# Kernel tuning notes

Measured on AMD Instinct MI355X. Metric: run time of the kernel, lower is better.

Reference implementation:

```python
import jax, jax.numpy as jnp
import numpy as np

B, SEED, GEN = 32, 128, 384
IN, H, OUT = 171, 1024, 171


def setup_inputs() -> dict:
    key = jax.random.key(0)
    ks = jax.random.split(key, 16)
    s = 0.05
    w = lambda k, shape: (jax.random.normal(k, shape, jnp.float32) * s)
    inp = {
        "seed_seq": jax.random.normal(ks[0], (B, SEED, IN), jnp.float32),
        "Wih1": w(ks[1], (4 * H, IN)),  "Whh1": w(ks[2], (4 * H, H)),
        "bih1": w(ks[3], (4 * H,)),     "bhh1": w(ks[4], (4 * H,)),
        "Wih2": w(ks[5], (4 * H, H)),   "Whh2": w(ks[6], (4 * H, H)),
        "bih2": w(ks[7], (4 * H,)),     "bhh2": w(ks[8], (4 * H,)),
        "Wih3": w(ks[9], (4 * H, H)),   "Whh3": w(ks[10], (4 * H, H)),
        "bih3": w(ks[11], (4 * H,)),    "bhh3": w(ks[12], (4 * H,)),
        "Wdec": w(ks[13], (OUT, H)),    "bdec": w(ks[14], (OUT,)),
        "gen_len": GEN,
    }
    return inp


def _lstm_cell(x, h, c, Wih, Whh, bih, bhh):
    # PyTorch LSTMCell: gate order i, f, g, o
    gates = x @ Wih.T + bih + h @ Whh.T + bhh  # [B, 4H]
    i, f, g, o = jnp.split(gates, 4, axis=-1)
    c_new = jax.nn.sigmoid(f) * c + jax.nn.sigmoid(i) * jnp.tanh(g)
    h_new = jax.nn.sigmoid(o) * jnp.tanh(c_new)
    return h_new, c_new


def reference(seed_seq, Wih1, Whh1, bih1, bhh1, Wih2, Whh2, bih2, bhh2,
              Wih3, Whh3, bih3, bhh3, Wdec, bdec, gen_len):
    batch = seed_seq.shape[0]
    hsz = Whh1.shape[1]
    z = jnp.zeros((batch, hsz), seed_seq.dtype)

    def step(state, x):
        h1, c1, h2, c2, h3, c3 = state
        h1, c1 = _lstm_cell(x, h1, c1, Wih1, Whh1, bih1, bhh1)
        h2, c2 = _lstm_cell(h1, h2, c2, Wih2, Whh2, bih2, bhh2)
        h3, c3 = _lstm_cell(h2, h3, c3, Wih3, Whh3, bih3, bhh3)
        out = h3 @ Wdec.T + bdec
        return (h1, c1, h2, c2, h3, c3), out

    # conditioning (seed) phase: scan over time-major seed sequence
    state0 = (z, z, z, z, z, z)
    state, seed_outs = jax.lax.scan(step, state0, jnp.swapaxes(seed_seq, 0, 1))

    def gen_step(carry, _):
        cur, st = carry
        st, out = step(st, cur)
        return (out, st), out

    _, gen_outs = jax.lax.scan(gen_step, (seed_outs[-1], state), None, length=gen_len)

    outs = jnp.concatenate([seed_outs, gen_outs], axis=0)  # [T, B, OUT]
    return jnp.swapaxes(outs, 0, 1)  # [B, T, OUT]
```

## Files before the change

### kernel.cpp

```cpp
#include <hip/hip_runtime.h>
#include <hip/hip_bf16.h>
#include <math.h>

#define NB    32
#define NSEED 128
#define NTT   512
#define NIN   171
#define NINP  192
#define NH    1024
#define NG    4096
#define NOUT  171
#define NOUTP 176
#define NWG   256

typedef unsigned short u16;
typedef unsigned int u32;
typedef __attribute__((ext_vector_type(8))) short bf16x8;
typedef __attribute__((ext_vector_type(4))) float f32x4;

__device__ __host__ inline u16 f2bf(float x) {
  union { float f; unsigned u; } v; v.f = x;
  unsigned r = v.u + 0x7FFFu + ((v.u >> 16) & 1u);
  return (u16)(r >> 16);
}

__global__ void pack_mat(const float* __restrict__ src, u16* __restrict__ dst, int ktiles) {
  int id = blockIdx.x * 256 + threadIdx.x;
  int total = ktiles * 256 * 64;
  if (id >= total) return;
  int lane = id & 63;
  int nt = (id >> 6) & 255;
  int kt = id >> 14;
  int c = lane & 15, q = lane >> 4;
  int r = (c & 3) * 1024 + nt * 4 + (c >> 2);
  int K = ktiles * 32;
  const float* s = src + (size_t)r * K + kt * 32 + q * 8;
  __attribute__((aligned(16))) u16 o[8];
#pragma unroll
  for (int j = 0; j < 8; ++j) o[j] = f2bf(s[j]);
  *(bf16x8*)(dst + (size_t)id * 8) = *(const bf16x8*)o;
}

__global__ void pack_wih1(const float* __restrict__ src, u16* __restrict__ dst) {
  int id = blockIdx.x * 256 + threadIdx.x;
  if (id >= 6 * 256 * 64) return;
  int lane = id & 63;
  int nt = (id >> 6) & 255;
  int kt = id >> 14;
  int c = lane & 15, q = lane >> 4;
  int r = (c & 3) * 1024 + nt * 4 + (c >> 2);
  int k0 = kt * 32 + q * 8;
  __attribute__((aligned(16))) u16 o[8];
#pragma unroll
  for (int j = 0; j < 8; ++j) {
    int k = k0 + j;
    o[j] = (k < NIN) ? f2bf(src[(size_t)r * NIN + k]) : (u16)0;
  }
  *(bf16x8*)(dst + (size_t)id * 8) = *(const bf16x8*)o;
}

__global__ void pack_wdec(const float* __restrict__ src, u16* __restrict__ dst) {
  int id = blockIdx.x * 256 + threadIdx.x;
  if (id >= 32 * 11 * 64) return;
  int lane = id & 63;
  int nt = (id >> 6) % 11;
  int kt = (id >> 6) / 11;
  int c = lane & 15, q = lane >> 4;
  int r = nt * 16 + c;
  int k0 = kt * 32 + q * 8;
  __attribute__((aligned(16))) u16 o[8];
#pragma unroll
  for (int j = 0; j < 8; ++j) {
    o[j] = (r < NOUT) ? f2bf(src[(size_t)r * NH + k0 + j]) : (u16)0;
  }
  *(bf16x8*)(dst + (size_t)id * 8) = *(const bf16x8*)o;
}

__global__ void pack_seed(const float* __restrict__ src, u16* __restrict__ dst) {
  int id = blockIdx.x * 256 + threadIdx.x;
  if (id >= NSEED * NB * NINP) return;
  int kp = id % NINP;
  int b = (id / NINP) % NB;
  int t = id / (NINP * NB);
  float v = (kp < NIN) ? src[((size_t)b * NSEED + t) * NIN + kp] : 0.f;
  dst[id] = f2bf(v);
}

__global__ void wfuse_kernel(const float* __restrict__ wih1, const float* __restrict__ wdec,
                             float* __restrict__ tmp) {
  int n = blockIdx.x;
  int k = blockIdx.y * 256 + threadIdx.x;
  const float* wr = wih1 + (size_t)n * NIN;
  float s = 0.f;
  for (int i = 0; i < NIN; ++i) s += wr[i] * wdec[(size_t)i * NH + k];
  tmp[(size_t)n * NH + k] = s;
}

__global__ void prep_bias(const float* bih1, const float* bhh1, const float* bih2, const float* bhh2,
                          const float* bih3, const float* bhh3, const float* __restrict__ wih1,
                          const float* __restrict__ bdec_in,
                          float* b1s, float* b1g, float* b2, float* b3, float* bdecp) {
  int n = blockIdx.x * 256 + threadIdx.x;
  if (n >= NG) return;
  int wgi = n >> 4, c = n & 15;
  int r = (c & 3) * 1024 + wgi * 4 + (c >> 2);
  float v1 = bih1[r] + bhh1[r];
  b1s[n] = v1;
  float bf = 0.f;
  for (int i = 0; i < NIN; ++i) bf += wih1[(size_t)r * NIN + i] * bdec_in[i];
  b1g[n] = v1 + bf;
  b2[n] = bih2[r] + bhh2[r];
  b3[n] = bih3[r] + bhh3[r];
  if (n < NOUTP) bdecp[n] = (n < NOUT) ? bdec_in[n] : 0.f;
}

__device__ __forceinline__ void load16_sc1(bf16x8 (&a0)[8], bf16x8 (&a1)[8],
                                           const u16* b0, const u16* b1) {
  asm volatile(
      "global_load_dwordx4 %0, %16, off sc0 sc1\n\t"
      "global_load_dwordx4 %8, %17, off sc0 sc1\n\t"
      "global_load_dwordx4 %1, %16, off offset:256 sc0 sc1\n\t"
      "global_load_dwordx4 %9, %17, off offset:256 sc0 sc1\n\t"
      "global_load_dwordx4 %2, %16, off offset:512 sc0 sc1\n\t"
      "global_load_dwordx4 %10, %17, off offset:512 sc0 sc1\n\t"
      "global_load_dwordx4 %3, %16, off offset:768 sc0 sc1\n\t"
      "global_load_dwordx4 %11, %17, off offset:768 sc0 sc1\n\t"
      "global_load_dwordx4 %4, %16, off offset:1024 sc0 sc1\n\t"
      "global_load_dwordx4 %12, %17, off offset:1024 sc0 sc1\n\t"
      "global_load_dwordx4 %5, %16, off offset:1280 sc0 sc1\n\t"
      "global_load_dwordx4 %13, %17, off offset:1280 sc0 sc1\n\t"
      "global_load_dwordx4 %6, %16, off offset:1536 sc0 sc1\n\t"
      "global_load_dwordx4 %14, %17, off offset:1536 sc0 sc1\n\t"
      "global_load_dwordx4 %7, %16, off offset:1792 sc0 sc1\n\t"
      "global_load_dwordx4 %15, %17, off offset:1792 sc0 sc1\n\t"
      "s_waitcnt vmcnt(0)"
      : "=&v"(a0[0]), "=&v"(a0[1]), "=&v"(a0[2]), "=&v"(a0[3]),
        "=&v"(a0[4]), "=&v"(a0[5]), "=&v"(a0[6]), "=&v"(a0[7]),
        "=&v"(a1[0]), "=&v"(a1[1]), "=&v"(a1[2]), "=&v"(a1[3]),
        "=&v"(a1[4]), "=&v"(a1[5]), "=&v"(a1[6]), "=&v"(a1[7])
      : "v"(b0), "v"(b1)
      : "memory");
}

#define MFMA_BF16 __builtin_amdgcn_mfma_f32_16x16x32_bf16

__device__ __forceinline__ void mm32_lds(f32x4& d0, f32x4& d1, const u16* wl,
                                         const u16* x, int wv, int lane) {
  int m = lane & 15, q = lane >> 4;
  const u16* xa = x + m * NH + q * 8 + wv * 32;
  const u16* xb = xa + 16 * NH;
  bf16x8 a0[8], a1[8];
  load16_sc1(a0, a1, xa, xb);
  const u16* wb = wl + lane * 8;
#pragma unroll
  for (int i = 0; i < 8; ++i) {
    bf16x8 w = *(const bf16x8*)(wb + (size_t)(wv + 4 * i) * 512);
    d0 = MFMA_BF16(a0[i], w, d0, 0, 0, 0);
    d1 = MFMA_BF16(a1[i], w, d1, 0, 0, 0);
  }
}

__device__ __forceinline__ void mm32_glb(f32x4& d0, f32x4& d1, const u16* wgb,
                                         const u16* x, int wv, int lane) {
  int m = lane & 15, q = lane >> 4;
  const u16* xa = x + m * NH + q * 8 + wv * 32;
  const u16* xb = xa + 16 * NH;
  const u16* wb = wgb + lane * 8;
  bf16x8 w[8];
#pragma unroll
  for (int i = 0; i < 8; ++i) w[i] = *(const bf16x8*)(wb + (size_t)(wv + 4 * i) * 131072);
  bf16x8 a0[8], a1[8];
  load16_sc1(a0, a1, xa, xb);
#pragma unroll
  for (int i = 0; i < 8; ++i) {
    d0 = MFMA_BF16(a0[i], w[i], d0, 0, 0, 0);
    d1 = MFMA_BF16(a1[i], w[i], d1, 0, 0, 0);
  }
}

__device__ __forceinline__ void mm6_glb(f32x4& d0, f32x4& d1, const u16* __restrict__ wbase,
                                        const u16* __restrict__ x, int wv, int lane) {
  int m = lane & 15, q = lane >> 4;
  const u16* xa = x + m * NINP + q * 8;
  const u16* xb = xa + 16 * NINP;
  const u16* wb = wbase + lane * 8;
#pragma unroll
  for (int i = 0; i < 2; ++i) {
    int kt = wv + 4 * i;
    if (kt >= 6) break;
    bf16x8 w = *(const bf16x8*)(wb + (size_t)kt * 131072);
    bf16x8 a0 = *(const bf16x8*)(xa + kt * 32);
    bf16x8 a1 = *(const bf16x8*)(xb + kt * 32);
    d0 = MFMA_BF16(a0, w, d0, 0, 0, 0);
    d1 = MFMA_BF16(a1, w, d1, 0, 0, 0);
  }
}

__global__ __launch_bounds__(256, 1) void lstm_main(
    const u16* __restrict__ whh1, const u16* __restrict__ whh2, const u16* __restrict__ whh3,
    const u16* __restrict__ wih2, const u16* __restrict__ wih3,
    const u16* __restrict__ wfuse, const u16* __restrict__ wih1,
    const u16* __restrict__ seedp,
    u16* __restrict__ h1b, u16* __restrict__ h2b, u16* __restrict__ h3h,
    const float* __restrict__ b1s, const float* __restrict__ b1g,
    const float* __restrict__ b2, const float* __restrict__ b3,
    int* __restrict__ flags)
{
  __shared__ u16  wlds[3 * 16384];
  __shared__ float red[4][64][8];
  __shared__ float gbuf[32][16];
  __shared__ float cst[3][32][4];

  int wg = blockIdx.x;
  int tid = threadIdx.x;
  int wv = tid >> 6, lane = tid & 63;

  {
    const u16* srcs[3] = { wih2 + (size_t)wg * 512, wih3 + (size_t)wg * 512,
                           wfuse + (size_t)wg * 512 };
#pragma unroll
    for (int m = 0; m < 3; ++m) {
      for (int i = tid; i < 2048; i += 256) {
        int kt = i >> 6, ln = i & 63;
        *(bf16x8*)&wlds[m * 16384 + (kt * 64 + ln) * 8] =
            *(const bf16x8*)(srcs[m] + ((size_t)kt * 16384 + ln) * 8);
      }
    }
    float* cp = &cst[0][0][0];
    for (int i = tid; i < 3 * 32 * 4; i += 256) cp[i] = 0.f;
  }
  __syncthreads();

  int c0 = tid & 15;
  float bv_s  = b1s[wg * 16 + c0];
  float bv_g  = b1g[wg * 16 + c0];
  float bv_2  = b2 [wg * 16 + c0];
  float bv_3  = b3 [wg * 16 + c0];

  const u16* whhg[3] = { whh1 + (size_t)wg * 512, whh2 + (size_t)wg * 512,
                         whh3 + (size_t)wg * 512 };
  const u16* wih1g = wih1 + (size_t)wg * 512;

  int ep = 0;
  for (int t = 0; t < NTT; ++t) {
    int par = t & 1, parp = par ^ 1;
    for (int l = 0; l < 3; ++l) {
      f32x4 d0 = {0.f, 0.f, 0.f, 0.f}, d1 = {0.f, 0.f, 0.f, 0.f};
      bool isseed = (t < NSEED);

      if (l == 0 && isseed)
        mm6_glb(d0, d1, wih1g, seedp + (size_t)t * NB * NINP, wv, lane);
      if (t > 0) {
        const u16* hs = (l == 0) ? h1b + (size_t)parp * NB * NH
                     : (l == 1) ? h2b + (size_t)parp * NB * NH
                                : h3h + (size_t)(t - 1) * NB * NH;
        mm32_glb(d0, d1, whhg[l], hs, wv, lane);
      }

      bool skipwait = (l == 0 && isseed);
      if (ep > 0 && !skipwait) {
        if (tid < 64) {
          const int* fp = flags + (tid << 2);
          for (;;) {
            int f0 = __hip_atomic_load(fp + 0, __ATOMIC_RELAXED, __HIP_MEMORY_SCOPE_AGENT);
            int f1 = __hip_atomic_load(fp + 1, __ATOMIC_RELAXED, __HIP_MEMORY_SCOPE_AGENT);
            int f2 = __hip_atomic_load(fp + 2, __ATOMIC_RELAXED, __HIP_MEMORY_SCOPE_AGENT);
            int f3 = __hip_atomic_load(fp + 3, __ATOMIC_RELAXED, __HIP_MEMORY_SCOPE_AGENT);
            int mn = min(min(f0, f1), min(f2, f3));
            if (__all(mn >= ep)) break;
            __builtin_amdgcn_s_sleep(1);
          }
        }
        __syncthreads();
      }

      if (l == 0) {
        if (!isseed)
          mm32_lds(d0, d1, &wlds[2 * 16384], h3h + (size_t)(t - 1) * NB * NH, wv, lane);
      } else {
        const u16* xs = (l == 1) ? h1b + (size_t)par * NB * NH
                                 : h2b + (size_t)par * NB * NH;
        mm32_lds(d0, d1, &wlds[(l - 1) * 16384], xs, wv, lane);
      }

#pragma unroll
      for (int r = 0; r < 4; ++r) { red[wv][lane][r] = d0[r]; red[wv][lane][4 + r] = d1[r]; }
      __syncthreads();
      {
        int c = tid & 15, brow = tid >> 4;
        float bv = (l == 0) ? (isseed ? bv_s : bv_g) : (l == 1) ? bv_2 : bv_3;
        int srcl = ((brow >> 2) << 4) | c;
#pragma unroll
        for (int mt = 0; mt < 2; ++mt) {
          int b = brow + mt * 16;
          int idx = mt * 4 + (brow & 3);
          gbuf[b][c] = red[0][srcl][idx] + red[1][srcl][idx] +
                       red[2][srcl][idx] + red[3][srcl][idx] + bv;
        }
      }
      __syncthreads();

      if (tid < 128) {
        int b = tid & 31, jl = tid >> 5;
        float gi = gbuf[b][jl * 4 + 0], gf = gbuf[b][jl * 4 + 1];
        float gg = gbuf[b][jl * 4 + 2], go = gbuf[b][jl * 4 + 3];
        float si = 1.f / (1.f + expf(-gi));
        float sf = 1.f / (1.f + expf(-gf));
        float so = 1.f / (1.f + expf(-go));
        float cn = sf * cst[l][b][jl] + si * tanhf(gg);
        cst[l][b][jl] = cn;
        float hn = so * tanhf(cn);
        unsigned hv = (unsigned)f2bf(hn);
        unsigned other = (unsigned)__shfl_xor((int)hv, 32, 64);
        if (lane < 32) {
          unsigned val = hv | (other << 16);
          int w01 = tid >> 6;
          u16* hdst = (l == 0) ? h1b + (size_t)par * NB * NH
                    : (l == 1) ? h2b + (size_t)par * NB * NH
                               : h3h + (size_t)t * NB * NH;
          u32* hp = (u32*)hdst + (size_t)b * 512 + wg * 2 + w01;
          __hip_atomic_store(hp, val, __ATOMIC_RELAXED, __HIP_MEMORY_SCOPE_AGENT);
        }
      }

      __syncthreads();
      ++ep;
      if (tid == 0)
        __hip_atomic_store(&flags[wg], ep, __ATOMIC_RELAXED, __HIP_MEMORY_SCOPE_AGENT);
    }
  }
}

__global__ __launch_bounds__(256) void dec_kernel(
    const u16* __restrict__ h3h, const u16* __restrict__ wdec,
    const float* __restrict__ bdecp, float* __restrict__ out)
{
  int task = blockIdx.x * 4 + (threadIdx.x >> 6);
  int lane = threadIdx.x & 63;
  int nt = task % 11, rt = task / 11;
  if (rt >= NTT) return;
  int m = lane & 15, q = lane >> 4;
  const u16* xa = h3h + ((size_t)rt * 32 + m) * NH + q * 8;
  const u16* xb = xa + (size_t)16 * NH;
  f32x4 d0 = {0.f, 0.f, 0.f, 0.f}, d1 = {0.f, 0.f, 0.f, 0.f};
  for (int kt = 0; kt < 32; ++kt) {
    bf16x8 bf = *(const bf16x8*)(wdec + ((size_t)(kt * 11 + nt) * 64 + lane) * 8);
    bf16x8 a0 = *(const bf16x8*)(xa + kt * 32);
    bf16x8 a1 = *(const bf16x8*)(xb + kt * 32);
    d0 = MFMA_BF16(a0, bf, d0, 0, 0, 0);
    d1 = MFMA_BF16(a1, bf, d1, 0, 0, 0);
  }
  int o = nt * 16 + m;
  if (o >= NOUT) return;
  float bv = bdecp[o];
#pragma unroll
  for (int reg = 0; reg < 4; ++reg) {
    int row0 = rt * 32 + q * 4 + reg;
    out[(((size_t)(row0 & 31)) * NTT + (row0 >> 5)) * NOUT + o] = d0[reg] + bv;
    int row1 = row0 + 16;
    out[(((size_t)(row1 & 31)) * NTT + (row1 >> 5)) * NOUT + o] = d1[reg] + bv;
  }
}

extern "C" void kernel_launch(void* const* d_in, const int* in_sizes, int n_in,
                              void* d_out, int out_size, void* d_ws, size_t ws_size,
                              hipStream_t stream) {
  const float* seed = (const float*)d_in[0];
  const float* Wih1 = (const float*)d_in[1];
  const float* Whh1 = (const float*)d_in[2];
  const float* bih1 = (const float*)d_in[3];
  const float* bhh1 = (const float*)d_in[4];
  const float* Wih2 = (const float*)d_in[5];
  const float* Whh2 = (const float*)d_in[6];
  const float* bih2 = (const float*)d_in[7];
  const float* bhh2 = (const float*)d_in[8];
  const float* Wih3 = (const float*)d_in[9];
  const float* Whh3 = (const float*)d_in[10];
  const float* bih3 = (const float*)d_in[11];
  const float* bhh3 = (const float*)d_in[12];
  const float* Wdec = (const float*)d_in[13];
  const float* bdec = (const float*)d_in[14];

  char* ws = (char*)d_ws;
  size_t off = 0;
  auto alloc = [&](size_t bytes) -> void* {
    void* p = ws + off;
    off += (bytes + 63) & ~(size_t)63;
    return p;
  };
  const size_t BIGPK = (size_t)32 * 256 * 64 * 8 * 2;
  u16* whh1p  = (u16*)alloc(BIGPK);
  u16* whh2p  = (u16*)alloc(BIGPK);
  u16* whh3p  = (u16*)alloc(BIGPK);
  u16* wih2p  = (u16*)alloc(BIGPK);
  u16* wih3p  = (u16*)alloc(BIGPK);
  u16* wfusep = (u16*)alloc(BIGPK);
  u16* wih1p  = (u16*)alloc((size_t)6 * 256 * 64 * 8 * 2);
  u16* wdecp  = (u16*)alloc((size_t)32 * 11 * 64 * 8 * 2);
  u16* seedp  = (u16*)alloc((size_t)NSEED * NB * NINP * 2);
  u16* h1b    = (u16*)alloc((size_t)2 * NB * NH * 2);
  u16* h2b    = (u16*)alloc((size_t)2 * NB * NH * 2);
  u16* h3h    = (u16*)alloc((size_t)NTT * NB * NH * 2);
  float* b1s  = (float*)alloc((size_t)NG * 4);
  float* b1g  = (float*)alloc((size_t)NG * 4);
  float* b2   = (float*)alloc((size_t)NG * 4);
  float* b3   = (float*)alloc((size_t)NG * 4);
  float* bdecp = (float*)alloc((size_t)NOUTP * 4);
  int* flags  = (int*)alloc((size_t)NWG * 4);
  float* wftmp = (float*)h3h;

  pack_mat<<<dim3(2048), dim3(256), 0, stream>>>(Whh1, whh1p, 32);
  pack_mat<<<dim3(2048), dim3(256), 0, stream>>>(Whh2, whh2p, 32);
  pack_mat<<<dim3(2048), dim3(256), 0, stream>>>(Whh3, whh3p, 32);
  pack_mat<<<dim3(2048), dim3(256), 0, stream>>>(Wih2, wih2p, 32);
  pack_mat<<<dim3(2048), dim3(256), 0, stream>>>(Wih3, wih3p, 32);
  pack_wih1<<<dim3(384), dim3(256), 0, stream>>>(Wih1, wih1p);
  wfuse_kernel<<<dim3(4096, 4), dim3(256), 0, stream>>>(Wih1, Wdec, wftmp);
  pack_mat<<<dim3(2048), dim3(256), 0, stream>>>(wftmp, wfusep, 32);
  pack_wdec<<<dim3(88), dim3(256), 0, stream>>>(Wdec, wdecp);
  pack_seed<<<dim3(3072), dim3(256), 0, stream>>>(seed, seedp);
  prep_bias<<<dim3(16), dim3(256), 0, stream>>>(bih1, bhh1, bih2, bhh2, bih3, bhh3,
                                                Wih1, bdec, b1s, b1g, b2, b3, bdecp);
  lstm_main<<<dim3(NWG), dim3(256), 0, stream>>>(
      whh1p, whh2p, whh3p, wih2p, wih3p, wfusep, wih1p, seedp,
      h1b, h2b, h3h, b1s, b1g, b2, b3, flags);
  dec_kernel<<<dim3(1408), dim3(256), 0, stream>>>(h3h, wdecp, bdecp, (float*)d_out);
}
```

Measured before the change: 8.179 ms.

## Use per-timestep hidden-state history so h loads can use normal caching

Replaces the double-buffered h1/h2 buffers with full per-timestep history buffers. Every hidden-state read then hits an address that has never been read before, so the inline-asm sc0 sc1 cache-bypassing loads can become ordinary cached vector loads, cutting latency on the serial recurrence path. It also swaps expf/tanhf gate math for fast exp and reciprocal approximations, issues the LDS weight loads before the MFMAs, and resets the sync flags in prep_bias. The costs are extra workspace memory and a reliance on never-reused addresses for cross-workgroup visibility without explicit cache bypass, plus slightly lower activation precision.

```diff
diff --git a/kernel.cpp b/kernel.cpp
--- a/kernel.cpp
+++ b/kernel.cpp
@@ -99,7 +99,8 @@
 __global__ void prep_bias(const float* bih1, const float* bhh1, const float* bih2, const float* bhh2,
                           const float* bih3, const float* bhh3, const float* __restrict__ wih1,
                           const float* __restrict__ bdec_in,
-                          float* b1s, float* b1g, float* b2, float* b3, float* bdecp) {
+                          float* b1s, float* b1g, float* b2, float* b3, float* bdecp,
+                          int* __restrict__ flags) {
   int n = blockIdx.x * 256 + threadIdx.x;
   if (n >= NG) return;
   int wgi = n >> 4, c = n & 15;
@@ -112,65 +113,53 @@
   b2[n] = bih2[r] + bhh2[r];
   b3[n] = bih3[r] + bhh3[r];
   if (n < NOUTP) bdecp[n] = (n < NOUT) ? bdec_in[n] : 0.f;
-}
-
-__device__ __forceinline__ void load16_sc1(bf16x8 (&a0)[8], bf16x8 (&a1)[8],
-                                           const u16* b0, const u16* b1) {
-  asm volatile(
-      "global_load_dwordx4 %0, %16, off sc0 sc1\n\t"
-      "global_load_dwordx4 %8, %17, off sc0 sc1\n\t"
-      "global_load_dwordx4 %1, %16, off offset:256 sc0 sc1\n\t"
-      "global_load_dwordx4 %9, %17, off offset:256 sc0 sc1\n\t"
-      "global_load_dwordx4 %2, %16, off offset:512 sc0 sc1\n\t"
-      "global_load_dwordx4 %10, %17, off offset:512 sc0 sc1\n\t"
-      "global_load_dwordx4 %3, %16, off offset:768 sc0 sc1\n\t"
-      "global_load_dwordx4 %11, %17, off offset:768 sc0 sc1\n\t"
-      "global_load_dwordx4 %4, %16, off offset:1024 sc0 sc1\n\t"
-      "global_load_dwordx4 %12, %17, off offset:1024 sc0 sc1\n\t"
-      "global_load_dwordx4 %5, %16, off offset:1280 sc0 sc1\n\t"
-      "global_load_dwordx4 %13, %17, off offset:1280 sc0 sc1\n\t"
-      "global_load_dwordx4 %6, %16, off offset:1536 sc0 sc1\n\t"
-      "global_load_dwordx4 %14, %17, off offset:1536 sc0 sc1\n\t"
-      "global_load_dwordx4 %7, %16, off offset:1792 sc0 sc1\n\t"
-      "global_load_dwordx4 %15, %17, off offset:1792 sc0 sc1\n\t"
-      "s_waitcnt vmcnt(0)"
-      : "=&v"(a0[0]), "=&v"(a0[1]), "=&v"(a0[2]), "=&v"(a0[3]),
-        "=&v"(a0[4]), "=&v"(a0[5]), "=&v"(a0[6]), "=&v"(a0[7]),
-        "=&v"(a1[0]), "=&v"(a1[1]), "=&v"(a1[2]), "=&v"(a1[3]),
-        "=&v"(a1[4]), "=&v"(a1[5]), "=&v"(a1[6]), "=&v"(a1[7])
-      : "v"(b0), "v"(b1)
-      : "memory");
+  if (n < NWG) flags[n] = 0;
+}
+
+__device__ __forceinline__ float fsig(float x) {
+  return __builtin_amdgcn_rcpf(1.f + __expf(-x));
+}
+__device__ __forceinline__ float ftanh(float x) {
+  return 1.f - 2.f * __builtin_amdgcn_rcpf(1.f + __expf(2.f * x));
 }
 
 #define MFMA_BF16 __builtin_amdgcn_mfma_f32_16x16x32_bf16
 
 __device__ __forceinline__ void mm32_lds(f32x4& d0, f32x4& d1, const u16* wl,
-                                         const u16* x, int wv, int lane) {
+                                         const u16* __restrict__ x, int wv, int lane) {
   int m = lane & 15, q = lane >> 4;
   const u16* xa = x + m * NH + q * 8 + wv * 32;
   const u16* xb = xa + 16 * NH;
-  bf16x8 a0[8], a1[8];
-  load16_sc1(a0, a1, xa, xb);
   const u16* wb = wl + lane * 8;
+  bf16x8 w[8], a0[8], a1[8];
+#pragma unroll
+  for (int i = 0; i < 8; ++i) w[i] = *(const bf16x8*)(wb + (size_t)(wv + 4 * i) * 512);
 #pragma unroll
   for (int i = 0; i < 8; ++i) {
-    bf16x8 w = *(const bf16x8*)(wb + (size_t)(wv + 4 * i) * 512);
-    d0 = MFMA_BF16(a0[i], w, d0, 0, 0, 0);
-    d1 = MFMA_BF16(a1[i], w, d1, 0, 0, 0);
-  }
-}
-
-__device__ __forceinline__ void mm32_glb(f32x4& d0, f32x4& d1, const u16* wgb,
-                                         const u16* x, int wv, int lane) {
+    a0[i] = *(const bf16x8*)(xa + i * 128);
+    a1[i] = *(const bf16x8*)(xb + i * 128);
+  }
+#pragma unroll
+  for (int i = 0; i < 8; ++i) {
+    d0 = MFMA_BF16(a0[i], w[i], d0, 0, 0, 0);
+    d1 = MFMA_BF16(a1[i], w[i], d1, 0, 0, 0);
+  }
+}
+
+__device__ __forceinline__ void mm32_glb(f32x4& d0, f32x4& d1, const u16* __restrict__ wgb,
+                                         const u16* __restrict__ x, int wv, int lane) {
   int m = lane & 15, q = lane >> 4;
   const u16* xa = x + m * NH + q * 8 + wv * 32;
   const u16* xb = xa + 16 * NH;
   const u16* wb = wgb + lane * 8;
-  bf16x8 w[8];
+  bf16x8 w[8], a0[8], a1[8];
 #pragma unroll
   for (int i = 0; i < 8; ++i) w[i] = *(const bf16x8*)(wb + (size_t)(wv + 4 * i) * 131072);
-  bf16x8 a0[8], a1[8];
-  load16_sc1(a0, a1, xa, xb);
+#pragma unroll
+  for (int i = 0; i < 8; ++i) {
+    a0[i] = *(const bf16x8*)(xa + i * 128);
+    a1[i] = *(const bf16x8*)(xb + i * 128);
+  }
 #pragma unroll
   for (int i = 0; i < 8; ++i) {
     d0 = MFMA_BF16(a0[i], w[i], d0, 0, 0, 0);
@@ -201,7 +190,7 @@
     const u16* __restrict__ wih2, const u16* __restrict__ wih3,
     const u16* __restrict__ wfuse, const u16* __restrict__ wih1,
     const u16* __restrict__ seedp,
-    u16* __restrict__ h1b, u16* __restrict__ h2b, u16* __restrict__ h3h,
+    u16* __restrict__ h1h, u16* __restrict__ h2h, u16* __restrict__ h3h,
     const float* __restrict__ b1s, const float* __restrict__ b1g,
     const float* __restrict__ b2, const float* __restrict__ b3,
     int* __restrict__ flags)
@@ -243,7 +232,6 @@
 
   int ep = 0;
   for (int t = 0; t < NTT; ++t) {
-    int par = t & 1, parp = par ^ 1;
     for (int l = 0; l < 3; ++l) {
       f32x4 d0 = {0.f, 0.f, 0.f, 0.f}, d1 = {0.f, 0.f, 0.f, 0.f};
       bool isseed = (t < NSEED);
@@ -251,8 +239,8 @@
       if (l == 0 && isseed)
         mm6_glb(d0, d1, wih1g, seedp + (size_t)t * NB * NINP, wv, lane);
       if (t > 0) {
-        const u16* hs = (l == 0) ? h1b + (size_t)parp * NB * NH
-                     : (l == 1) ? h2b + (size_t)parp * NB * NH
+        const u16* hs = (l == 0) ? h1h + (size_t)(t - 1) * NB * NH
+                     : (l == 1) ? h2h + (size_t)(t - 1) * NB * NH
                                 : h3h + (size_t)(t - 1) * NB * NH;
         mm32_glb(d0, d1, whhg[l], hs, wv, lane);
       }
@@ -278,8 +266,8 @@
         if (!isseed)
           mm32_lds(d0, d1, &wlds[2 * 16384], h3h + (size_t)(t - 1) * NB * NH, wv, lane);
       } else {
-        const u16* xs = (l == 1) ? h1b + (size_t)par * NB * NH
-                                 : h2b + (size_t)par * NB * NH;
+        const u16* xs = (l == 1) ? h1h + (size_t)t * NB * NH
+                                 : h2h + (size_t)t * NB * NH;
         mm32_lds(d0, d1, &wlds[(l - 1) * 16384], xs, wv, lane);
       }
 
@@ -304,19 +292,19 @@
         int b = tid & 31, jl = tid >> 5;
         float gi = gbuf[b][jl * 4 + 0], gf = gbuf[b][jl * 4 + 1];
         float gg = gbuf[b][jl * 4 + 2], go = gbuf[b][jl * 4 + 3];
-        float si = 1.f / (1.f + expf(-gi));
-        float sf = 1.f / (1.f + expf(-gf));
-        float so = 1.f / (1.f + expf(-go));
-        float cn = sf * cst[l][b][jl] + si * tanhf(gg);
+        float si = fsig(gi);
+        float sf = fsig(gf);
+        float so = fsig(go);
+        float cn = sf * cst[l][b][jl] + si * ftanh(gg);
         cst[l][b][jl] = cn;
-        float hn = so * tanhf(cn);
+        float hn = so * ftanh(cn);
         unsigned hv = (unsigned)f2bf(hn);
         unsigned other = (unsigned)__shfl_xor((int)hv, 32, 64);
         if (lane < 32) {
           unsigned val = hv | (other << 16);
           int w01 = tid >> 6;
-          u16* hdst = (l == 0) ? h1b + (size_t)par * NB * NH
-                    : (l == 1) ? h2b + (size_t)par * NB * NH
+          u16* hdst = (l == 0) ? h1h + (size_t)t * NB * NH
+                    : (l == 1) ? h2h + (size_t)t * NB * NH
                                : h3h + (size_t)t * NB * NH;
           u32* hp = (u32*)hdst + (size_t)b * 512 + wg * 2 + w01;
           __hip_atomic_store(hp, val, __ATOMIC_RELAXED, __HIP_MEMORY_SCOPE_AGENT);
@@ -389,6 +377,7 @@
     return p;
   };
   const size_t BIGPK = (size_t)32 * 256 * 64 * 8 * 2;
+  const size_t HHIST = (size_t)NTT * NB * NH * 2;
   u16* whh1p  = (u16*)alloc(BIGPK);
   u16* whh2p  = (u16*)alloc(BIGPK);
   u16* whh3p  = (u16*)alloc(BIGPK);
@@ -398,9 +387,9 @@
   u16* wih1p  = (u16*)alloc((size_t)6 * 256 * 64 * 8 * 2);
   u16* wdecp  = (u16*)alloc((size_t)32 * 11 * 64 * 8 * 2);
   u16* seedp  = (u16*)alloc((size_t)NSEED * NB * NINP * 2);
-  u16* h1b    = (u16*)alloc((size_t)2 * NB * NH * 2);
-  u16* h2b    = (u16*)alloc((size_t)2 * NB * NH * 2);
-  u16* h3h    = (u16*)alloc((size_t)NTT * NB * NH * 2);
+  u16* h1h    = (u16*)alloc(HHIST);
+  u16* h2h    = (u16*)alloc(HHIST);
+  u16* h3h    = (u16*)alloc(HHIST);
   float* b1s  = (float*)alloc((size_t)NG * 4);
   float* b1g  = (float*)alloc((size_t)NG * 4);
   float* b2   = (float*)alloc((size_t)NG * 4);
@@ -420,9 +409,9 @@
   pack_wdec<<<dim3(88), dim3(256), 0, stream>>>(Wdec, wdecp);
   pack_seed<<<dim3(3072), dim3(256), 0, stream>>>(seed, seedp);
   prep_bias<<<dim3(16), dim3(256), 0, stream>>>(bih1, bhh1, bih2, bhh2, bih3, bhh3,
-                                                Wih1, bdec, b1s, b1g, b2, b3, bdecp);
+                                                Wih1, bdec, b1s, b1g, b2, b3, bdecp, flags);
   lstm_main<<<dim3(NWG), dim3(256), 0, stream>>>(
       whh1p, whh2p, whh3p, wih2p, wih3p, wfusep, wih1p, seedp,
-      h1b, h2b, h3h, b1s, b1g, b2, b3, flags);
+      h1h, h2h, h3h, b1s, b1g, b2, b3, flags);
   dec_kernel<<<dim3(1408), dim3(256), 0, stream>>>(h3h, wdecp, bdecp, (float*)d_out);
 }
```

New measurement: 7.976 ms. 1.03x faster.
